# Optimization experiments

Measured on AMD Instinct MI355X. Metric: run time of the kernel, lower is better.

Reference implementation:

```python
import jax, jax.numpy as jnp
import numpy as np


def setup_inputs() -> dict:
    key = jax.random.key(0)
    k1, k2, k3, k4 = jax.random.split(key, 4)
    B, C = 32768, 10
    x = jax.random.normal(k1, (B, 1, 28, 28), dtype=jnp.float32)
    linear_weight = jax.random.normal(k2, (4 * 14 * 14 + 1 + 2, C), dtype=jnp.float32)
    linear_bias = jax.random.normal(k3, (C,), dtype=jnp.float32)
    sampler_weights = jax.random.normal(k4, (4,), dtype=jnp.float32)
    return {"x": x, "linear_weight": linear_weight, "linear_bias": linear_bias,
            "sampler_weights": sampler_weights}


def reference(x, linear_weight, linear_bias, sampler_weights):
    # Closed-form simulation of the 4-qubit circuits:
    # RY(t)|0> -> <Z>=cos(t); after CX(0,1): <Z1> = cos(t0)*cos(t1); CX(2,3) likewise.
    B = x.shape[0]
    # Extract non-overlapping 2x2 patches in row-major order -> (B, 196, 4)
    p = x[:, 0].reshape(B, 14, 2, 14, 2).transpose(0, 1, 3, 2, 4).reshape(B, 196, 4)
    c = jnp.cos(p)
    # quanvolution_circuit per patch: [cos a, cos a cos b, cos c, cos c cos d]
    feats = jnp.stack([c[..., 0], c[..., 0] * c[..., 1],
                       c[..., 2], c[..., 2] * c[..., 3]], axis=-1)  # (B,196,4)
    qfeat = feats.reshape(B, 784)
    # fully_connected_circuit on qfeat[:, :4]: mean of the four post-CX <Z>
    cf = jnp.cos(qfeat[:, :4])
    qfc = (cf[:, 0] + cf[:, 0] * cf[:, 1] + cf[:, 2] + cf[:, 2] * cf[:, 3]) / 4.0  # (B,)
    # sampler_circuit: sequential RY angles add on wires 0 and 1
    t0 = qfeat[:, 0] + sampler_weights[0] + sampler_weights[2]
    t1 = qfeat[:, 1] + sampler_weights[1] + sampler_weights[3]
    z0 = jnp.cos(t0)
    z1 = z0 * jnp.cos(t1)
    sampler = jax.nn.softmax(jnp.stack([z0, z1], axis=-1), axis=-1)  # (B,2)
    combined = jnp.concatenate([qfeat, qfc[:, None], sampler], axis=-1)  # (B,787)
    logits = combined @ linear_weight + linear_bias
    return jax.nn.log_softmax(logits, axis=-1)
```

## Files before the change

### kernel.cpp

```cpp
#include <hip/hip_runtime.h>


__global__ __launch_bounds__(256, 2)
void qml_kernel(const float* __restrict__ x,
                const float* __restrict__ w,
                const float* __restrict__ bias,
                const float* __restrict__ sw,
                float* __restrict__ out,
                int B)
{
    const int lane = threadIdx.x & 63;
    const int sub = __builtin_amdgcn_readfirstlane((int)(threadIdx.x >> 6));

    int sample = blockIdx.x * 64 + lane;
    const bool active = (sample < B);
    if (sample >= B) sample = B - 1;

    const float* __restrict__ xrow = x + (size_t)sample * 784;

    float acc[10];
#pragma unroll
    for (int c = 0; c < 10; ++c) acc[c] = 0.0f;

    float qf0 = 0.f, qf1 = 0.f, qf2 = 0.f, qf3 = 0.f;

    int i = 0, j = sub;
    int wofs = 40 * sub;

    for (int q = 0; q < 49; ++q) {
        const int off = (2 * i) * 28 + 2 * j;
        const float2 a01 = *(const float2*)(xrow + off);
        const float2 a23 = *(const float2*)(xrow + off + 28);

        const float c0 = __cosf(a01.x);
        const float c1 = __cosf(a01.y);
        const float c2 = __cosf(a23.x);
        const float c3 = __cosf(a23.y);
        const float v0 = c0;
        const float v1 = c0 * c1;
        const float v2 = c2;
        const float v3 = c2 * c3;

        if (sub == 0 && q == 0) { qf0 = v0; qf1 = v1; qf2 = v2; qf3 = v3; }

        const float* __restrict__ wr = w + wofs;
#pragma unroll
        for (int c = 0; c < 10; ++c) {
            acc[c] += v0 * wr[c] + v1 * wr[10 + c] + v2 * wr[20 + c] + v3 * wr[30 + c];
        }

        wofs += 160;
        j += 4;
        if (j >= 14) { j -= 14; i += 1; }
    }

    __shared__ float red[3][64][10];
    if (sub != 0) {
#pragma unroll
        for (int c = 0; c < 10; ++c) red[sub - 1][lane][c] = acc[c];
    }
    __syncthreads();

    if (sub == 0) {
#pragma unroll
        for (int c = 0; c < 10; ++c)
            acc[c] += red[0][lane][c] + red[1][lane][c] + red[2][lane][c];

        const float cf0 = __cosf(qf0);
        const float cf1 = __cosf(qf1);
        const float cf2 = __cosf(qf2);
        const float cf3 = __cosf(qf3);
        const float qfc = (cf0 + cf0 * cf1 + cf2 + cf2 * cf3) * 0.25f;

        const float t0 = qf0 + sw[0] + sw[2];
        const float t1 = qf1 + sw[1] + sw[3];
        const float z0 = __cosf(t0);
        const float z1 = z0 * __cosf(t1);
        const float e0 = __expf(z0);
        const float e1 = __expf(z1);
        const float inv = 1.0f / (e0 + e1);
        const float s0 = e0 * inv;
        const float s1 = e1 * inv;

        const float* __restrict__ wt = w + 7840;
#pragma unroll
        for (int c = 0; c < 10; ++c)
            acc[c] += qfc * wt[c] + s0 * wt[10 + c] + s1 * wt[20 + c] + bias[c];

        float m = acc[0];
#pragma unroll
        for (int c = 1; c < 10; ++c) m = fmaxf(m, acc[c]);
        float ssum = 0.0f;
#pragma unroll
        for (int c = 0; c < 10; ++c) ssum += __expf(acc[c] - m);
        const float lse = __logf(ssum) + m;

        if (active) {
            float* __restrict__ orow = out + (size_t)sample * 10;
#pragma unroll
            for (int c = 0; c < 10; ++c) orow[c] = acc[c] - lse;
        }
    }
}

extern "C" void kernel_launch(void* const* d_in, const int* in_sizes, int n_in,
                              void* d_out, int out_size, void* d_ws, size_t ws_size,
                              hipStream_t stream) {
    const float* x    = (const float*)d_in[0];
    const float* w    = (const float*)d_in[1];
    const float* bias = (const float*)d_in[2];
    const float* sw   = (const float*)d_in[3];
    float* out = (float*)d_out;

    const int B = in_sizes[0] / 784;
    const int blocks = (B + 63) / 64;
    qml_kernel<<<blocks, 256, 0, stream>>>(x, w, bias, sw, out, B);
}
```

Baseline: 174.3 us.

## Split each sample's image rows across 14 waves and parallelize epilogue per logit

```diff
diff --git a/kernel.cpp b/kernel.cpp
--- a/kernel.cpp
+++ b/kernel.cpp
@@ -1,19 +1,26 @@
 #include <hip/hip_runtime.h>
 
 
-__global__ __launch_bounds__(256, 2)
+#define NWAVES 14
+#define BLOCKT (NWAVES * 64)
+
+__global__ __launch_bounds__(BLOCKT, 7)
 void qml_kernel(const float* __restrict__ x,
-                const float* __restrict__ w,
+                const float* __restrict__ wm,
                 const float* __restrict__ bias,
                 const float* __restrict__ sw,
                 float* __restrict__ out,
                 int B)
 {
+    __shared__ float red[NWAVES][64 * 11];
+    __shared__ float qfs[64 * 5];
+    __shared__ float lg[64 * 11];
+
     const int lane = threadIdx.x & 63;
-    const int sub = __builtin_amdgcn_readfirstlane((int)(threadIdx.x >> 6));
+    const int wv = __builtin_amdgcn_readfirstlane((int)(threadIdx.x >> 6));
 
     int sample = blockIdx.x * 64 + lane;
-    const bool active = (sample < B);
+    const bool s_ok = (sample < B);
     if (sample >= B) sample = B - 1;
 
     const float* __restrict__ xrow = x + (size_t)sample * 784;
@@ -22,84 +29,87 @@
 #pragma unroll
     for (int c = 0; c < 10; ++c) acc[c] = 0.0f;
 
+    const int rowoff = 56 * wv;
+    const float* __restrict__ wbase = wm + (size_t)rowoff * 10;
+
     float qf0 = 0.f, qf1 = 0.f, qf2 = 0.f, qf3 = 0.f;
 
-    int i = 0, j = sub;
-    int wofs = 40 * sub;
+#pragma unroll
+    for (int k = 0; k < 7; ++k) {
+        const float4 top = *(const float4*)(xrow + rowoff + 4 * k);
+        const float4 bot = *(const float4*)(xrow + rowoff + 28 + 4 * k);
 
-    for (int q = 0; q < 49; ++q) {
-        const int off = (2 * i) * 28 + 2 * j;
-        const float2 a01 = *(const float2*)(xrow + off);
-        const float2 a23 = *(const float2*)(xrow + off + 28);
+        const float ca = __cosf(top.x), cb = __cosf(top.y);
+        const float cc = __cosf(bot.x), cd = __cosf(bot.y);
+        const float vA0 = ca, vA1 = ca * cb, vA2 = cc, vA3 = cc * cd;
 
-        const float c0 = __cosf(a01.x);
-        const float c1 = __cosf(a01.y);
-        const float c2 = __cosf(a23.x);
-        const float c3 = __cosf(a23.y);
-        const float v0 = c0;
-        const float v1 = c0 * c1;
-        const float v2 = c2;
-        const float v3 = c2 * c3;
+        const float ce = __cosf(top.z), cf = __cosf(top.w);
+        const float cg = __cosf(bot.z), ch = __cosf(bot.w);
+        const float vB0 = ce, vB1 = ce * cf, vB2 = cg, vB3 = cg * ch;
 
-        if (sub == 0 && q == 0) { qf0 = v0; qf1 = v1; qf2 = v2; qf3 = v3; }
+        if (wv == 0 && k == 0) { qf0 = vA0; qf1 = vA1; qf2 = vA2; qf3 = vA3; }
 
-        const float* __restrict__ wr = w + wofs;
+        const float* __restrict__ wr = wbase + 80 * k;
 #pragma unroll
         for (int c = 0; c < 10; ++c) {
-            acc[c] += v0 * wr[c] + v1 * wr[10 + c] + v2 * wr[20 + c] + v3 * wr[30 + c];
+            acc[c] += vA0 * wr[c]      + vA1 * wr[10 + c]
+                    + vA2 * wr[20 + c] + vA3 * wr[30 + c]
+                    + vB0 * wr[40 + c] + vB1 * wr[50 + c]
+                    + vB2 * wr[60 + c] + vB3 * wr[70 + c];
         }
-
-        wofs += 160;
-        j += 4;
-        if (j >= 14) { j -= 14; i += 1; }
     }
 
-    __shared__ float red[3][64][10];
-    if (sub != 0) {
 #pragma unroll
-        for (int c = 0; c < 10; ++c) red[sub - 1][lane][c] = acc[c];
+    for (int c = 0; c < 10; ++c) red[wv][lane * 11 + c] = acc[c];
+    if (wv == 0) {
+        qfs[lane * 5 + 0] = qf0; qfs[lane * 5 + 1] = qf1;
+        qfs[lane * 5 + 2] = qf2; qfs[lane * 5 + 3] = qf3;
     }
     __syncthreads();
 
-    if (sub == 0) {
+    const int t = threadIdx.x;
+    const int s = t / 10;
+    const int c = t - 10 * s;
+    float logit = 0.0f;
+
+    if (t < 640) {
+        float sum = 0.0f;
 #pragma unroll
-        for (int c = 0; c < 10; ++c)
-            acc[c] += red[0][lane][c] + red[1][lane][c] + red[2][lane][c];
+        for (int w2 = 0; w2 < NWAVES; ++w2) sum += red[w2][s * 11 + c];
 
-        const float cf0 = __cosf(qf0);
-        const float cf1 = __cosf(qf1);
-        const float cf2 = __cosf(qf2);
-        const float cf3 = __cosf(qf3);
-        const float qfc = (cf0 + cf0 * cf1 + cf2 + cf2 * cf3) * 0.25f;
+        const float q0 = qfs[s * 5 + 0], q1 = qfs[s * 5 + 1];
+        const float q2 = qfs[s * 5 + 2], q3 = qfs[s * 5 + 3];
 
-        const float t0 = qf0 + sw[0] + sw[2];
-        const float t1 = qf1 + sw[1] + sw[3];
+        const float f0 = __cosf(q0), f1 = __cosf(q1);
+        const float f2 = __cosf(q2), f3 = __cosf(q3);
+        const float qfc = (f0 + f0 * f1 + f2 + f2 * f3) * 0.25f;
+
+        const float t0 = q0 + sw[0] + sw[2];
+        const float t1 = q1 + sw[1] + sw[3];
         const float z0 = __cosf(t0);
         const float z1 = z0 * __cosf(t1);
         const float e0 = __expf(z0);
         const float e1 = __expf(z1);
         const float inv = 1.0f / (e0 + e1);
-        const float s0 = e0 * inv;
-        const float s1 = e1 * inv;
+        const float s0 = e0 * inv, s1 = e1 * inv;
 
-        const float* __restrict__ wt = w + 7840;
+        const float* __restrict__ wt = wm + 7840;
+        logit = sum + bias[c] + qfc * wt[c] + s0 * wt[10 + c] + s1 * wt[20 + c];
+        lg[s * 11 + c] = logit;
+    }
+    __syncthreads();
+
+    if (t < 640) {
+        float m = -3.4e38f;
 #pragma unroll
-        for (int c = 0; c < 10; ++c)
-            acc[c] += qfc * wt[c] + s0 * wt[10 + c] + s1 * wt[20 + c] + bias[c];
-
-        float m = acc[0];
-#pragma unroll
-        for (int c = 1; c < 10; ++c) m = fmaxf(m, acc[c]);
+        for (int k2 = 0; k2 < 10; ++k2) m = fmaxf(m, lg[s * 11 + k2]);
         float ssum = 0.0f;
 #pragma unroll
-        for (int c = 0; c < 10; ++c) ssum += __expf(acc[c] - m);
+        for (int k2 = 0; k2 < 10; ++k2) ssum += __expf(lg[s * 11 + k2] - m);
         const float lse = __logf(ssum) + m;
 
-        if (active) {
-            float* __restrict__ orow = out + (size_t)sample * 10;
-#pragma unroll
-            for (int c = 0; c < 10; ++c) orow[c] = acc[c] - lse;
-        }
+        if (blockIdx.x * 64 + s < B)
+            out[(size_t)blockIdx.x * 640 + t] = logit - lse;
     }
 }
 
@@ -114,5 +124,5 @@
 
     const int B = in_sizes[0] / 784;
     const int blocks = (B + 63) / 64;
-    qml_kernel<<<blocks, 256, 0, stream>>>(x, w, bias, sw, out, B);
+    qml_kernel<<<blocks, BLOCKT, 0, stream>>>(x, w, bias, sw, out, B);
 }
```

Result: slower. 297.0 us (+70.4%).
